# Kernel tuning notes

Measured on AMD Instinct MI355X. Metric: run time of the kernel, lower is better.

The kernel has to match this reference:

```python
import jax, jax.numpy as jnp
import numpy as np

N_CELLS = 8_388_608   # total flattened cells across all subdomains (~4096x2048 global grid)
N_HALO = 1_048_576    # total halo (boundary) destination cells across all subdomain edges
N_Q = 12              # raw field quantities: u, v, b_u, b_v, h, H, hh, dif_h, eta1, k_u, k_v, k3


def setup_inputs() -> dict:
    key = jax.random.key(0)
    k1, k2, k3 = jax.random.split(key, 3)
    fields = jax.random.normal(k1, (N_Q, N_CELLS), dtype=jnp.float32)
    # precomputed gather map: each halo cell reads up to 2 source cells
    src_idx = jax.random.randint(k2, (N_HALO, 2), 0, N_CELLS, dtype=jnp.int32)
    # ratio map: coarse->fine (ratio 0.5, repeat_interleave) = copy [1,0];
    # fine->coarse (ratio 2, mean over group of 2) = [0.5,0.5]; ratio 1 = copy [1,0]
    coarse = jax.random.bernoulli(k3, 0.5, (N_HALO,))
    weights = jnp.where(coarse[:, None],
                        jnp.array([0.5, 0.5], dtype=jnp.float32),
                        jnp.array([1.0, 0.0], dtype=jnp.float32))
    return {"fields": fields, "src_idx": src_idx, "weights": weights}


def reference(fields, src_idx, weights):
    # unpack raw quantities
    u, v, b_u, b_v, h, Hb, hh, dif_h, eta1, k_u, k_v, k3 = fields
    # derived boundary quantities exchanged by update_halos (11 halo buffers)
    derived = jnp.stack([
        u, v, b_u, b_v, h, hh, dif_h,
        h + Hb,                    # halo_eta
        eta1,                      # halo_eta1
        jnp.minimum(k_u, k3),      # halo_k_uu
        jnp.minimum(k_v, k3),      # halo_k_vv
    ])  # [11, N_CELLS]
    # batched gather-rescale-scatter: halo[q, e] = sum_j weights[e, j] * derived[q, src_idx[e, j]]
    gathered = derived[:, src_idx]                     # [11, E, 2]
    halos = jnp.einsum('qej,ej->qe', gathered, weights)  # [11, E]
    return halos
```

## Files before the change

kernel.cpp:

```cpp
#include <hip/hip_runtime.h>

#define N_CELLS 8388608
#define N_HALO  1048576

__global__ __launch_bounds__(256) void halo_gather_kernel(
    const float* __restrict__ fields,
    const int2*  __restrict__ src_idx,
    const float2* __restrict__ weights,
    float* __restrict__ out)
{
    const int e = blockIdx.x * blockDim.x + threadIdx.x;
    if (e >= N_HALO) return;

    const int2   ij = src_idx[e];
    const float2 wv = weights[e];

    const size_t i0 = (size_t)ij.x;
    const size_t i1 = (size_t)ij.y;

    float a[12];
    float b[12];

    #pragma unroll
    for (int q = 0; q < 12; ++q)
        a[q] = fields[(size_t)q * N_CELLS + i0];

    #pragma unroll
    for (int q = 0; q < 12; ++q) b[q] = 0.0f;
    if (wv.y != 0.0f) {
        #pragma unroll
        for (int q = 0; q < 12; ++q)
            b[q] = fields[(size_t)q * N_CELLS + i1];
    }

    const float w0 = wv.x, w1 = wv.y;

    float r[11];
    r[0]  = a[0] * w0 + b[0] * w1;
    r[1]  = a[1] * w0 + b[1] * w1;
    r[2]  = a[2] * w0 + b[2] * w1;
    r[3]  = a[3] * w0 + b[3] * w1;
    r[4]  = a[4] * w0 + b[4] * w1;
    r[5]  = a[6] * w0 + b[6] * w1;
    r[6]  = a[7] * w0 + b[7] * w1;
    r[7]  = (a[4] + a[5]) * w0 + (b[4] + b[5]) * w1;
    r[8]  = a[8] * w0 + b[8] * w1;
    r[9]  = fminf(a[9],  a[11]) * w0 + fminf(b[9],  b[11]) * w1;
    r[10] = fminf(a[10], a[11]) * w0 + fminf(b[10], b[11]) * w1;

    #pragma unroll
    for (int q = 0; q < 11; ++q)
        out[(size_t)q * N_HALO + e] = r[q];
}

extern "C" void kernel_launch(void* const* d_in, const int* in_sizes, int n_in,
                              void* d_out, int out_size, void* d_ws, size_t ws_size,
                              hipStream_t stream) {
    const float*  fields  = (const float*)d_in[0];
    const int2*   src_idx = (const int2*)d_in[1];
    const float2* weights = (const float2*)d_in[2];
    float* out = (float*)d_out;

    const int block = 256;
    const int grid  = (N_HALO + block - 1) / block;
    halo_gather_kernel<<<grid, block, 0, stream>>>(fields, src_idx, weights, out);
}
```

Baseline: 806.3 us.

## Split halo gather into four kernels over field subsets for cache locality

Splits the single gather kernel into four launches, each reading three field rows and writing the outputs that depend on them. This shrinks the random-access working set per pass so gathered cache lines can be reused from the large last-level cache instead of refetched from HBM. In exchange, indices and weights are reread four times and three extra kernel launches are added.

```diff
diff --git a/kernel.cpp b/kernel.cpp
--- a/kernel.cpp
+++ b/kernel.cpp
@@ -3,54 +3,87 @@
 #define N_CELLS 8388608
 #define N_HALO  1048576
 
-__global__ __launch_bounds__(256) void halo_gather_kernel(
-    const float* __restrict__ fields,
-    const int2*  __restrict__ src_idx,
-    const float2* __restrict__ weights,
-    float* __restrict__ out)
+
+__device__ __forceinline__ void load_pair(const float* __restrict__ row,
+                                          size_t i0, size_t i1, bool has2,
+                                          float& a, float& b) {
+    a = row[i0];
+    b = has2 ? row[i1] : 0.0f;
+}
+
+__global__ __launch_bounds__(256) void g1(
+    const float* __restrict__ fields, const int2* __restrict__ src_idx,
+    const float2* __restrict__ weights, float* __restrict__ out)
 {
     const int e = blockIdx.x * blockDim.x + threadIdx.x;
     if (e >= N_HALO) return;
+    const int2 ij = src_idx[e];
+    const float2 wv = weights[e];
+    const size_t i0 = (size_t)ij.x, i1 = (size_t)ij.y;
+    const bool has2 = (wv.y != 0.0f);
+    float a0,b0,a1,b1,a2,b2;
+    load_pair(fields + 0ull*N_CELLS, i0, i1, has2, a0, b0);
+    load_pair(fields + 1ull*N_CELLS, i0, i1, has2, a1, b1);
+    load_pair(fields + 2ull*N_CELLS, i0, i1, has2, a2, b2);
+    out[0ull*N_HALO + e] = a0*wv.x + b0*wv.y;
+    out[1ull*N_HALO + e] = a1*wv.x + b1*wv.y;
+    out[2ull*N_HALO + e] = a2*wv.x + b2*wv.y;
+}
 
-    const int2   ij = src_idx[e];
+__global__ __launch_bounds__(256) void g2(
+    const float* __restrict__ fields, const int2* __restrict__ src_idx,
+    const float2* __restrict__ weights, float* __restrict__ out)
+{
+    const int e = blockIdx.x * blockDim.x + threadIdx.x;
+    if (e >= N_HALO) return;
+    const int2 ij = src_idx[e];
     const float2 wv = weights[e];
+    const size_t i0 = (size_t)ij.x, i1 = (size_t)ij.y;
+    const bool has2 = (wv.y != 0.0f);
+    float a3,b3,a4,b4,a5,b5;
+    load_pair(fields + 3ull*N_CELLS, i0, i1, has2, a3, b3);
+    load_pair(fields + 4ull*N_CELLS, i0, i1, has2, a4, b4);
+    load_pair(fields + 5ull*N_CELLS, i0, i1, has2, a5, b5);
+    out[3ull*N_HALO + e] = a3*wv.x + b3*wv.y;
+    out[4ull*N_HALO + e] = a4*wv.x + b4*wv.y;
+    out[7ull*N_HALO + e] = (a4 + a5)*wv.x + (b4 + b5)*wv.y;
+}
 
-    const size_t i0 = (size_t)ij.x;
-    const size_t i1 = (size_t)ij.y;
+__global__ __launch_bounds__(256) void g3(
+    const float* __restrict__ fields, const int2* __restrict__ src_idx,
+    const float2* __restrict__ weights, float* __restrict__ out)
+{
+    const int e = blockIdx.x * blockDim.x + threadIdx.x;
+    if (e >= N_HALO) return;
+    const int2 ij = src_idx[e];
+    const float2 wv = weights[e];
+    const size_t i0 = (size_t)ij.x, i1 = (size_t)ij.y;
+    const bool has2 = (wv.y != 0.0f);
+    float a6,b6,a7,b7,a8,b8;
+    load_pair(fields + 6ull*N_CELLS, i0, i1, has2, a6, b6);
+    load_pair(fields + 7ull*N_CELLS, i0, i1, has2, a7, b7);
+    load_pair(fields + 8ull*N_CELLS, i0, i1, has2, a8, b8);
+    out[5ull*N_HALO + e] = a6*wv.x + b6*wv.y;
+    out[6ull*N_HALO + e] = a7*wv.x + b7*wv.y;
+    out[8ull*N_HALO + e] = a8*wv.x + b8*wv.y;
+}
 
-    float a[12];
-    float b[12];
-
-    #pragma unroll
-    for (int q = 0; q < 12; ++q)
-        a[q] = fields[(size_t)q * N_CELLS + i0];
-
-    #pragma unroll
-    for (int q = 0; q < 12; ++q) b[q] = 0.0f;
-    if (wv.y != 0.0f) {
-        #pragma unroll
-        for (int q = 0; q < 12; ++q)
-            b[q] = fields[(size_t)q * N_CELLS + i1];
-    }
-
-    const float w0 = wv.x, w1 = wv.y;
-
-    float r[11];
-    r[0]  = a[0] * w0 + b[0] * w1;
-    r[1]  = a[1] * w0 + b[1] * w1;
-    r[2]  = a[2] * w0 + b[2] * w1;
-    r[3]  = a[3] * w0 + b[3] * w1;
-    r[4]  = a[4] * w0 + b[4] * w1;
-    r[5]  = a[6] * w0 + b[6] * w1;
-    r[6]  = a[7] * w0 + b[7] * w1;
-    r[7]  = (a[4] + a[5]) * w0 + (b[4] + b[5]) * w1;
-    r[8]  = a[8] * w0 + b[8] * w1;
-    r[9]  = fminf(a[9],  a[11]) * w0 + fminf(b[9],  b[11]) * w1;
-    r[10] = fminf(a[10], a[11]) * w0 + fminf(b[10], b[11]) * w1;
-
-    #pragma unroll
-    for (int q = 0; q < 11; ++q)
-        out[(size_t)q * N_HALO + e] = r[q];
+__global__ __launch_bounds__(256) void g4(
+    const float* __restrict__ fields, const int2* __restrict__ src_idx,
+    const float2* __restrict__ weights, float* __restrict__ out)
+{
+    const int e = blockIdx.x * blockDim.x + threadIdx.x;
+    if (e >= N_HALO) return;
+    const int2 ij = src_idx[e];
+    const float2 wv = weights[e];
+    const size_t i0 = (size_t)ij.x, i1 = (size_t)ij.y;
+    const bool has2 = (wv.y != 0.0f);
+    float a9,b9,a10,b10,a11,b11;
+    load_pair(fields +  9ull*N_CELLS, i0, i1, has2, a9,  b9);
+    load_pair(fields + 10ull*N_CELLS, i0, i1, has2, a10, b10);
+    load_pair(fields + 11ull*N_CELLS, i0, i1, has2, a11, b11);
+    out[ 9ull*N_HALO + e] = fminf(a9,  a11)*wv.x + fminf(b9,  b11)*wv.y;
+    out[10ull*N_HALO + e] = fminf(a10, a11)*wv.x + fminf(b10, b11)*wv.y;
 }
 
 extern "C" void kernel_launch(void* const* d_in, const int* in_sizes, int n_in,
@@ -63,5 +96,8 @@
 
     const int block = 256;
     const int grid  = (N_HALO + block - 1) / block;
-    halo_gather_kernel<<<grid, block, 0, stream>>>(fields, src_idx, weights, out);
+    g1<<<grid, block, 0, stream>>>(fields, src_idx, weights, out);
+    g2<<<grid, block, 0, stream>>>(fields, src_idx, weights, out);
+    g3<<<grid, block, 0, stream>>>(fields, src_idx, weights, out);
+    g4<<<grid, block, 0, stream>>>(fields, src_idx, weights, out);
 }
```

Result: faster. 788.4 us (-2.2%).

## Pack fields into per-cell AoS workspace before halo gather

Applied to the files above, without the earlier changes.

Adds a pre-pass that transposes the 12 field planes into a 16-float per-cell record in the workspace, with the derived quantities (h+H, min with k3) computed during packing. The gather kernel then reads each source cell with three contiguous float4 loads instead of twelve scattered scalar loads. This trades a full streaming pass over all cells, with extra write traffic, for far fewer random memory transactions in the gather.

```diff
diff --git a/kernel.cpp b/kernel.cpp
--- a/kernel.cpp
+++ b/kernel.cpp
@@ -2,12 +2,29 @@
 
 #define N_CELLS 8388608
 #define N_HALO  1048576
+#define STRIDE  16
 
-__global__ __launch_bounds__(256) void halo_gather_kernel(
-    const float* __restrict__ fields,
-    const int2*  __restrict__ src_idx,
-    const float2* __restrict__ weights,
-    float* __restrict__ out)
+__global__ __launch_bounds__(256) void pack_kernel(
+    const float* __restrict__ fields, float* __restrict__ ws)
+{
+    const int c = blockIdx.x * blockDim.x + threadIdx.x;
+    if (c >= N_CELLS) return;
+
+    float f[12];
+    #pragma unroll
+    for (int q = 0; q < 12; ++q)
+        f[q] = fields[(size_t)q * N_CELLS + c];
+
+    float4* o = (float4*)(ws + (size_t)c * STRIDE);
+    o[0] = make_float4(f[0], f[1], f[2], f[3]);
+    o[1] = make_float4(f[4], f[6], f[7], f[4] + f[5]);
+    o[2] = make_float4(f[8], fminf(f[9], f[11]), fminf(f[10], f[11]), 0.0f);
+    o[3] = make_float4(0.0f, 0.0f, 0.0f, 0.0f);
+}
+
+__global__ __launch_bounds__(256) void gather_kernel(
+    const float* __restrict__ ws, const int2* __restrict__ src_idx,
+    const float2* __restrict__ weights, float* __restrict__ out)
 {
     const int e = blockIdx.x * blockDim.x + threadIdx.x;
     if (e >= N_HALO) return;
@@ -15,42 +32,27 @@
     const int2   ij = src_idx[e];
     const float2 wv = weights[e];
 
-    const size_t i0 = (size_t)ij.x;
-    const size_t i1 = (size_t)ij.y;
+    const float4* p0 = (const float4*)(ws + (size_t)ij.x * STRIDE);
+    float4 a0 = p0[0], a1 = p0[1], a2 = p0[2];
 
-    float a[12];
-    float b[12];
-
-    #pragma unroll
-    for (int q = 0; q < 12; ++q)
-        a[q] = fields[(size_t)q * N_CELLS + i0];
-
-    #pragma unroll
-    for (int q = 0; q < 12; ++q) b[q] = 0.0f;
+    float4 b0 = make_float4(0,0,0,0), b1 = b0, b2 = b0;
     if (wv.y != 0.0f) {
-        #pragma unroll
-        for (int q = 0; q < 12; ++q)
-            b[q] = fields[(size_t)q * N_CELLS + i1];
+        const float4* p1 = (const float4*)(ws + (size_t)ij.y * STRIDE);
+        b0 = p1[0]; b1 = p1[1]; b2 = p1[2];
     }
 
     const float w0 = wv.x, w1 = wv.y;
-
-    float r[11];
-    r[0]  = a[0] * w0 + b[0] * w1;
-    r[1]  = a[1] * w0 + b[1] * w1;
-    r[2]  = a[2] * w0 + b[2] * w1;
-    r[3]  = a[3] * w0 + b[3] * w1;
-    r[4]  = a[4] * w0 + b[4] * w1;
-    r[5]  = a[6] * w0 + b[6] * w1;
-    r[6]  = a[7] * w0 + b[7] * w1;
-    r[7]  = (a[4] + a[5]) * w0 + (b[4] + b[5]) * w1;
-    r[8]  = a[8] * w0 + b[8] * w1;
-    r[9]  = fminf(a[9],  a[11]) * w0 + fminf(b[9],  b[11]) * w1;
-    r[10] = fminf(a[10], a[11]) * w0 + fminf(b[10], b[11]) * w1;
-
-    #pragma unroll
-    for (int q = 0; q < 11; ++q)
-        out[(size_t)q * N_HALO + e] = r[q];
+    out[0ull*N_HALO + e]  = a0.x*w0 + b0.x*w1;
+    out[1ull*N_HALO + e]  = a0.y*w0 + b0.y*w1;
+    out[2ull*N_HALO + e]  = a0.z*w0 + b0.z*w1;
+    out[3ull*N_HALO + e]  = a0.w*w0 + b0.w*w1;
+    out[4ull*N_HALO + e]  = a1.x*w0 + b1.x*w1;
+    out[5ull*N_HALO + e]  = a1.y*w0 + b1.y*w1;
+    out[6ull*N_HALO + e]  = a1.z*w0 + b1.z*w1;
+    out[7ull*N_HALO + e]  = a1.w*w0 + b1.w*w1;
+    out[8ull*N_HALO + e]  = a2.x*w0 + b2.x*w1;
+    out[9ull*N_HALO + e]  = a2.y*w0 + b2.y*w1;
+    out[10ull*N_HALO + e] = a2.z*w0 + b2.z*w1;
 }
 
 extern "C" void kernel_launch(void* const* d_in, const int* in_sizes, int n_in,
@@ -60,8 +62,9 @@
     const int2*   src_idx = (const int2*)d_in[1];
     const float2* weights = (const float2*)d_in[2];
     float* out = (float*)d_out;
+    float* ws  = (float*)d_ws;
 
     const int block = 256;
-    const int grid  = (N_HALO + block - 1) / block;
-    halo_gather_kernel<<<grid, block, 0, stream>>>(fields, src_idx, weights, out);
+    pack_kernel  <<<(N_CELLS + block - 1) / block, block, 0, stream>>>(fields, ws);
+    gather_kernel<<<(N_HALO  + block - 1) / block, block, 0, stream>>>(ws, src_idx, weights, out);
 }
```

After: 759.1 us. -5.9%, faster.
